# Kernel tuning notes

Hardware: AMD Instinct MI355X
Metric: run time of the kernel (lower is better)

Reference implementation:

```python
import jax, jax.numpy as jnp
import numpy as np

B, C, H, W = 8, 256, 64, 64

def setup_inputs() -> dict:
    key = jax.random.key(0)
    ks = jax.random.split(key, 8)
    s = 0.05  # keep 1x1-conv outputs well-scaled
    return {
        "x": jax.random.normal(ks[0], (B, C, H, W), jnp.float32),
        "Wq": jax.random.normal(ks[1], (C, C), jnp.float32) * s,
        "bq": jax.random.normal(ks[2], (C,), jnp.float32) * s,
        "Wk": jax.random.normal(ks[3], (C, C), jnp.float32) * s,
        "bk": jax.random.normal(ks[4], (C,), jnp.float32) * s,
        "Wv": jax.random.normal(ks[5], (C, C), jnp.float32) * s,
        "bv": jax.random.normal(ks[6], (C,), jnp.float32) * s,
        "gamma": jax.random.normal(ks[7], (1,), jnp.float32),
    }

def reference(x, Wq, bq, Wk, bk, Wv, bv, gamma):
    bs, ch, w, h = x.shape
    n = w * h
    xf = x.reshape(bs, ch, n)                                  # (B, C, N)
    # 1x1 convs == per-position channel matmuls
    q = jnp.einsum('oc,bcn->bon', Wq, xf) + bq[None, :, None]  # (B, C, N)
    k = jnp.einsum('oc,bcn->bon', Wk, xf) + bk[None, :, None]
    v = jnp.einsum('oc,bcn->bon', Wv, xf) + bv[None, :, None]
    # energy[b,i,j] = <q[:,i], k[:,j]>
    energy = jnp.einsum('bci,bcj->bij', q, k)                  # (B, N, N)
    # NOTE: unusual post-softmax scaling by 1/sqrt(N), as in the source
    attn = jax.nn.softmax(energy, axis=-1) / jnp.sqrt(jnp.asarray(n, x.dtype))
    # out[b,c,i] = sum_j v[b,c,j] * attn[b,i,j]
    out = jnp.einsum('bcj,bij->bci', v, attn).reshape(bs, ch, w, h)
    return gamma[0] * out + x
```

## Files before the change

### kernel.cpp

```cpp
#include <hip/hip_runtime.h>

#define B_ 8
#define C_ 256
#define N_ 4096

typedef __attribute__((ext_vector_type(8))) __bf16 bf16x8;
typedef __attribute__((ext_vector_type(4))) float f32x4;

__device__ __forceinline__ unsigned short f2bf(float f) {
  union { float f; unsigned u; } v; v.f = f;
  unsigned r = v.u + 0x7fffu + ((v.u >> 16) & 1u);
  return (unsigned short)(r >> 16);
}

__device__ __forceinline__ uint4 pack8(const float* s) {
  uint4 o;
  o.x = (unsigned)f2bf(s[0]) | ((unsigned)f2bf(s[1]) << 16);
  o.y = (unsigned)f2bf(s[2]) | ((unsigned)f2bf(s[3]) << 16);
  o.z = (unsigned)f2bf(s[4]) | ((unsigned)f2bf(s[5]) << 16);
  o.w = (unsigned)f2bf(s[6]) | ((unsigned)f2bf(s[7]) << 16);
  return o;
}

__device__ __forceinline__ void dma16(const void* g, void* l) {
  __builtin_amdgcn_global_load_lds(
      (const __attribute__((address_space(1))) unsigned int*)(uintptr_t)g,
      (__attribute__((address_space(3))) unsigned int*)(uintptr_t)l, 16, 0, 0);
}

__global__ __launch_bounds__(256) void prep(
    const float* __restrict__ x,
    const float* __restrict__ Wq, const float* __restrict__ Wk,
    const float* __restrict__ Wv,
    unsigned short* __restrict__ xT, unsigned short* __restrict__ Wbf)
{
  __shared__ unsigned int xTl[64][33];
  const int t   = threadIdx.x;
  const int n0  = blockIdx.x * 64;
  const int ct0 = blockIdx.y * 64;
  const int b   = blockIdx.z;

  if (blockIdx.z == 0) {
    const int bid = blockIdx.x + 64 * blockIdx.y;
    if (bid < 96) {
      const int el0 = (bid * 256 + t) * 8;
      const int mat = el0 >> 16;
      const int off = el0 & 65535;
      const float* src = (mat == 0) ? Wq : (mat == 1) ? Wk : Wv;
      float tmp[8];
      float4 f0 = ((const float4*)(src + off))[0];
      float4 f1 = ((const float4*)(src + off))[1];
      tmp[0]=f0.x; tmp[1]=f0.y; tmp[2]=f0.z; tmp[3]=f0.w;
      tmp[4]=f1.x; tmp[5]=f1.y; tmp[6]=f1.z; tmp[7]=f1.w;
      *(uint4*)(Wbf + el0) = pack8(tmp);
    }
  }

  {
    const int cp = t >> 3;
    const int nq = t & 7;
    const float* s0 = x + ((size_t)(b * C_ + ct0 + 2*cp) * N_ + n0 + nq * 8);
    const float* s1 = s0 + N_;
    float4 a0 = ((const float4*)s0)[0], a1 = ((const float4*)s0)[1];
    float4 b0 = ((const float4*)s1)[0], b1 = ((const float4*)s1)[1];
    float lo[8] = {a0.x,a0.y,a0.z,a0.w,a1.x,a1.y,a1.z,a1.w};
    float hi[8] = {b0.x,b0.y,b0.z,b0.w,b1.x,b1.y,b1.z,b1.w};
    #pragma unroll
    for (int k = 0; k < 8; ++k)
      xTl[nq*8 + k][cp] = (unsigned)f2bf(lo[k]) | ((unsigned)f2bf(hi[k]) << 16);
  }
  __syncthreads();

  {
    const int n = t >> 2, cq = t & 3;
    unsigned int vals[8];
    #pragma unroll
    for (int g = 0; g < 8; ++g) vals[g] = xTl[n][cq*8 + g];
    uint4* dst = (uint4*)(xT + ((size_t)(b * N_ + n0 + n)) * C_ + ct0 + cq*16);
    dst[0] = make_uint4(vals[0], vals[1], vals[2], vals[3]);
    dst[1] = make_uint4(vals[4], vals[5], vals[6], vals[7]);
  }
}

__global__ __launch_bounds__(256, 2) void qkv_gemm(
    const unsigned short* __restrict__ xT, const unsigned short* __restrict__ Wbf,
    const float* __restrict__ bq, const float* __restrict__ bk,
    const float* __restrict__ bv,
    unsigned short* __restrict__ qT, unsigned short* __restrict__ kT,
    unsigned short* __restrict__ vW)
{
  __shared__ char smraw[49152];

  const int t    = threadIdx.x;
  const int lane = t & 63;
  const int w    = t >> 6;
  const int m16  = lane & 15;
  const int q    = (lane >> 4) & 3;
  const int nt0  = blockIdx.x * 128;
  const int b    = blockIdx.y;
  const int mat  = blockIdx.z;
  const size_t bN = (size_t)b * N_;

  const unsigned short* Wm = Wbf + mat * 65536;
  const float* bm = (mat == 0) ? bq : (mat == 1) ? bk : bv;
  unsigned short* outp = (mat == 0) ? qT : (mat == 1) ? kT : vW;

  auto stage = [&](int buf, int cs) {
    #pragma unroll
    for (int p = 0; p < 4; ++p) {
      const int row = 64 * w + 16 * p + (lane >> 2);
      const int g   = (lane & 3) ^ (row & 3);
      dma16(Wm + row * 256 + cs * 32 + g * 8,
            smraw + buf * 16384 + (64 * w + 16 * p) * 64);
    }
    #pragma unroll
    for (int p = 0; p < 2; ++p) {
      const int row = 32 * w + 16 * p + (lane >> 2);
      const int g   = (lane & 3) ^ (row & 3);
      dma16(xT + (bN + nt0 + row) * 256 + cs * 32 + g * 8,
            smraw + 32768 + buf * 8192 + (32 * w + 16 * p) * 64);
    }
  };

  stage(0, 0);

  float br[4][4];
  #pragma unroll
  for (int ob = 0; ob < 4; ++ob)
    #pragma unroll
    for (int r = 0; r < 4; ++r) br[ob][r] = bm[64*w + ob*16 + q*4 + r];

  f32x4 acc[4][8] = {};

  for (int cs = 0; cs < 8; ++cs) {
    asm volatile("s_waitcnt vmcnt(0)" ::: "memory");
    __syncthreads();
    if (cs + 1 < 8) stage((cs + 1) & 1, cs + 1);
    const int buf = cs & 1;
    const unsigned short* Wt = (const unsigned short*)(smraw + buf * 16384);
    const unsigned short* Xt = (const unsigned short*)(smraw + 32768 + buf * 8192);

    bf16x8 af[4], bf_[8];
    #pragma unroll
    for (int ob = 0; ob < 4; ++ob) {
      const int o = 64*w + ob*16 + m16;
      af[ob] = *(const bf16x8*)&Wt[o * 32 + ((q ^ (o & 3)) * 8)];
    }
    #pragma unroll
    for (int nb = 0; nb < 8; ++nb) {
      const int n = nb*16 + m16;
      bf_[nb] = *(const bf16x8*)&Xt[n * 32 + ((q ^ (n & 3)) * 8)];
    }
    #pragma unroll
    for (int ob = 0; ob < 4; ++ob)
      #pragma unroll
      for (int nb = 0; nb < 8; ++nb)
        acc[ob][nb] = __builtin_amdgcn_mfma_f32_16x16x32_bf16(af[ob], bf_[nb], acc[ob][nb], 0,0,0);
  }

  float* Dst = (float*)smraw;
  for (int nc = 0; nc < 4; ++nc) {
    __syncthreads();
    #pragma unroll
    for (int ob = 0; ob < 4; ++ob)
      #pragma unroll
      for (int h = 0; h < 2; ++h) {
        const int nb = nc*2 + h;
        #pragma unroll
        for (int r = 0; r < 4; ++r)
          Dst[(64*w + ob*16 + q*4 + r) * 36 + h*16 + m16] = acc[ob][nb][r] + br[ob][r];
      }
    __syncthreads();

    if (mat < 2) {
      const int n_loc = t & 31, oc = t >> 5;
      float vals[32];
      #pragma unroll
      for (int k = 0; k < 32; ++k) vals[k] = Dst[(oc*32 + k) * 36 + n_loc];
      uint4* dst = (uint4*)(outp + (bN + nt0 + nc*32 + n_loc) * C_ + oc*32);
      #pragma unroll
      for (int g = 0; g < 4; ++g) dst[g] = pack8(vals + g*8);
    } else {
      float vals[32], pv[32];
      #pragma unroll
      for (int k = 0; k < 32; ++k) vals[k] = Dst[t * 36 + k];
      #pragma unroll
      for (int p = 0; p < 32; ++p)
        pv[p] = vals[16*((p>>2)&1) + 4*(p>>3) + (p&3)];
      uint4* dst = (uint4*)(outp + ((size_t)(b * C_ + t)) * N_ + nt0 + nc*32);
      #pragma unroll
      for (int g = 0; g < 4; ++g) dst[g] = pack8(pv + g*8);
    }
  }
}

__global__ __launch_bounds__(256, 1) void attn8(
    const unsigned short* __restrict__ qT, const unsigned short* __restrict__ kT,
    const unsigned short* __restrict__ vW, const float* __restrict__ x,
    const float* __restrict__ gamma, float* __restrict__ out)
{
  __shared__ unsigned short Kbuf[2][32 * 256];
  __shared__ unsigned short Vbuf[3][256 * 32];

  const int t    = threadIdx.x;
  const int lane = t & 63;
  const int w    = t >> 6;
  const int b    = blockIdx.x;
  const int i0   = blockIdx.y * 128;
  const int m16  = lane & 15;
  const int q    = (lane >> 4) & 3;
  const int q8   = q * 8;
  const size_t bN = (size_t)b * N_;
  const size_t bC = (size_t)b * C_;

  auto stageK = [&](int buf, int j0) {
    #pragma unroll
    for (int p = 0; p < 4; ++p) {
      const int row = 8*w + 2*p + (lane >> 5);
      const int g   = (lane & 31) ^ (row & 7);
      dma16(kT + (bN + j0 + row) * C_ + g * 8, &Kbuf[buf][(8*w + 2*p) * 256]);
    }
  };
  auto stageV = [&](int buf, int j0) {
    #pragma unroll
    for (int p = 0; p < 4; ++p) {
      const int row = 64*w + 16*p + (lane >> 2);
      const int g   = (lane & 3) ^ ((row >> 1) & 3);
      dma16(vW + (bC + row) * N_ + j0 + g * 8, &Vbuf[buf][(64*w + 16*p) * 32]);
    }
  };

  stageK(0, 0); stageV(0, 0);

  bf16x8 qfA[8], qfB[8];
  {
    const unsigned short* qa = qT + ((bN + i0 + w*32 + m16) * C_ + q8);
    const unsigned short* qb = qa + 16 * C_;
    #pragma unroll
    for (int ks = 0; ks < 8; ++ks) {
      qfA[ks] = *(const bf16x8*)(qa + ks*32);
      qfB[ks] = *(const bf16x8*)(qb + ks*32);
    }
  }

  float lA = 0.0f, lB = 0.0f;
  f32x4 OA[16] = {}, OB[16] = {};
  uint4 pkA, pkB;
  int vb_prev = 0;

  {
    asm volatile("s_waitcnt vmcnt(0)" ::: "memory");
    __syncthreads();
    stageK(1, 32); stageV(1, 32);
    const unsigned short* Kt = Kbuf[0];

    f32x4 sA[2] = {}, sB[2] = {};
    __builtin_amdgcn_s_setprio(1);
    #pragma unroll
    for (int ks = 0; ks < 8; ++ks)
      #pragma unroll
      for (int jb = 0; jb < 2; ++jb) {
        const int j = jb*16 + m16;
        bf16x8 a = *(const bf16x8*)&Kt[j * 256 + (((4*ks + q) ^ (j & 7)) * 8)];
        sA[jb] = __builtin_amdgcn_mfma_f32_16x16x32_bf16(a, qfA[ks], sA[jb], 0,0,0);
        sB[jb] = __builtin_amdgcn_mfma_f32_16x16x32_bf16(a, qfB[ks], sB[jb], 0,0,0);
      }
    __builtin_amdgcn_s_setprio(0);

    float psA[2][4], psB[2][4];
    #pragma unroll
    for (int jb = 0; jb < 2; ++jb)
      #pragma unroll
      for (int r = 0; r < 4; ++r) {
        const float pa = __expf(sA[jb][r] - 64.0f);
        const float pb = __expf(sB[jb][r] - 64.0f);
        psA[jb][r] = pa; lA += pa;
        psB[jb][r] = pb; lB += pb;
      }
    pkA.x = (unsigned)f2bf(psA[0][0]) | ((unsigned)f2bf(psA[0][1]) << 16);
    pkA.y = (unsigned)f2bf(psA[0][2]) | ((unsigned)f2bf(psA[0][3]) << 16);
    pkA.z = (unsigned)f2bf(psA[1][0]) | ((unsigned)f2bf(psA[1][1]) << 16);
    pkA.w = (unsigned)f2bf(psA[1][2]) | ((unsigned)f2bf(psA[1][3]) << 16);
    pkB.x = (unsigned)f2bf(psB[0][0]) | ((unsigned)f2bf(psB[0][1]) << 16);
    pkB.y = (unsigned)f2bf(psB[0][2]) | ((unsigned)f2bf(psB[0][3]) << 16);
    pkB.z = (unsigned)f2bf(psB[1][0]) | ((unsigned)f2bf(psB[1][1]) << 16);
    pkB.w = (unsigned)f2bf(psB[1][2]) | ((unsigned)f2bf(psB[1][3]) << 16);
  }

  for (int jt = 1; jt < 128; ++jt) {
    asm volatile("s_waitcnt vmcnt(0)" ::: "memory");
    __syncthreads();
    const int vb_cur = (vb_prev == 2) ? 0 : vb_prev + 1;
    const int vb_nxt = (vb_cur == 2) ? 0 : vb_cur + 1;
    if (jt + 1 < 128) { stageK((jt + 1) & 1, (jt + 1) * 32); stageV(vb_nxt, (jt + 1) * 32); }

    const unsigned short* Kt = Kbuf[jt & 1];
    const unsigned short* Vp = Vbuf[vb_prev];
    union { uint4 u; bf16x8 v; } pva; pva.u = pkA;
    union { uint4 u; bf16x8 v; } pvb; pvb.u = pkB;

    f32x4 sA[2] = {}, sB[2] = {};
    __builtin_amdgcn_s_setprio(1);
    #pragma unroll
    for (int u = 0; u < 16; ++u) {
      {
        const int ks = u >> 1, jb = u & 1;
        const int j = jb*16 + m16;
        bf16x8 a = *(const bf16x8*)&Kt[j * 256 + (((4*ks + q) ^ (j & 7)) * 8)];
        sA[jb] = __builtin_amdgcn_mfma_f32_16x16x32_bf16(a, qfA[ks], sA[jb], 0,0,0);
        sB[jb] = __builtin_amdgcn_mfma_f32_16x16x32_bf16(a, qfB[ks], sB[jb], 0,0,0);
      }
      {
        const int c = u*16 + m16;
        bf16x8 vf = *(const bf16x8*)&Vp[c * 32 + ((q ^ ((c >> 1) & 3)) * 8)];
        OA[u] = __builtin_amdgcn_mfma_f32_16x16x32_bf16(vf, pva.v, OA[u], 0,0,0);
        OB[u] = __builtin_amdgcn_mfma_f32_16x16x32_bf16(vf, pvb.v, OB[u], 0,0,0);
      }
    }
    __builtin_amdgcn_s_setprio(0);

    float psA[2][4], psB[2][4];
    #pragma unroll
    for (int jb = 0; jb < 2; ++jb)
      #pragma unroll
      for (int r = 0; r < 4; ++r) {
        const float pa = __expf(sA[jb][r] - 64.0f);
        const float pb = __expf(sB[jb][r] - 64.0f);
        psA[jb][r] = pa; lA += pa;
        psB[jb][r] = pb; lB += pb;
      }
    pkA.x = (unsigned)f2bf(psA[0][0]) | ((unsigned)f2bf(psA[0][1]) << 16);
    pkA.y = (unsigned)f2bf(psA[0][2]) | ((unsigned)f2bf(psA[0][3]) << 16);
    pkA.z = (unsigned)f2bf(psA[1][0]) | ((unsigned)f2bf(psA[1][1]) << 16);
    pkA.w = (unsigned)f2bf(psA[1][2]) | ((unsigned)f2bf(psA[1][3]) << 16);
    pkB.x = (unsigned)f2bf(psB[0][0]) | ((unsigned)f2bf(psB[0][1]) << 16);
    pkB.y = (unsigned)f2bf(psB[0][2]) | ((unsigned)f2bf(psB[0][3]) << 16);
    pkB.z = (unsigned)f2bf(psB[1][0]) | ((unsigned)f2bf(psB[1][1]) << 16);
    pkB.w = (unsigned)f2bf(psB[1][2]) | ((unsigned)f2bf(psB[1][3]) << 16);
    vb_prev = vb_cur;
  }

  {
    const unsigned short* Vp = Vbuf[vb_prev];
    union { uint4 u; bf16x8 v; } pva; pva.u = pkA;
    union { uint4 u; bf16x8 v; } pvb; pvb.u = pkB;
    __builtin_amdgcn_s_setprio(1);
    #pragma unroll
    for (int cb = 0; cb < 16; ++cb) {
      const int c = cb*16 + m16;
      bf16x8 vf = *(const bf16x8*)&Vp[c * 32 + ((q ^ ((c >> 1) & 3)) * 8)];
      OA[cb] = __builtin_amdgcn_mfma_f32_16x16x32_bf16(vf, pva.v, OA[cb], 0,0,0);
      OB[cb] = __builtin_amdgcn_mfma_f32_16x16x32_bf16(vf, pvb.v, OB[cb], 0,0,0);
    }
    __builtin_amdgcn_s_setprio(0);
  }

  float lAs = lA;
  lAs += __shfl_xor(lAs, 16);
  lAs += __shfl_xor(lAs, 32);
  float lBs = lB;
  lBs += __shfl_xor(lBs, 16);
  lBs += __shfl_xor(lBs, 32);

  const float gm = gamma[0];
  const float fsA = gm / (lAs * 64.0f);
  const float fsB = gm / (lBs * 64.0f);
  const int icolA = i0 + w*32 + m16;
  const int icolB = icolA + 16;
  #pragma unroll
  for (int cb = 0; cb < 16; ++cb) {
    #pragma unroll
    for (int r = 0; r < 4; ++r) {
      const int c = cb*16 + q*4 + r;
      const size_t idxA = (bC + c) * N_ + icolA;
      out[idxA] = OA[cb][r] * fsA + x[idxA];
      const size_t idxB = idxA + 16;
      out[idxB] = OB[cb][r] * fsB + x[idxB];
    }
  }
}

extern "C" void kernel_launch(void* const* d_in, const int* in_sizes, int n_in,
                              void* d_out, int out_size, void* d_ws, size_t ws_size,
                              hipStream_t stream) {
  const float* x     = (const float*)d_in[0];
  const float* Wq    = (const float*)d_in[1];
  const float* bq    = (const float*)d_in[2];
  const float* Wk    = (const float*)d_in[3];
  const float* bk    = (const float*)d_in[4];
  const float* Wv    = (const float*)d_in[5];
  const float* bv    = (const float*)d_in[6];
  const float* gamma = (const float*)d_in[7];
  float* out = (float*)d_out;

  unsigned short* xT  = (unsigned short*)d_ws;
  unsigned short* Wbf = xT + (size_t)B_ * N_ * C_;
  unsigned short* qT  = Wbf + 3 * 65536;
  unsigned short* kT  = qT + (size_t)B_ * N_ * C_;
  unsigned short* vW  = kT + (size_t)B_ * N_ * C_;

  prep<<<dim3(64, 4, 8), dim3(256), 0, stream>>>(x, Wq, Wk, Wv, xT, Wbf);
  qkv_gemm<<<dim3(32, 8, 3), dim3(256), 0, stream>>>(xT, Wbf, bq, bk, bv, qT, kT, vW);
  attn8<<<dim3(8, 32), dim3(256), 0, stream>>>(qT, kT, vW, x, gamma, out);
}
```

Measured before the change: 331.8 us.

## Split attention key range across two blocks with atomic-flag partial reduction

Splits the key/value loop of each query tile into two halves handled by separate blocks, doubling the grid and allowing two blocks per CU. The first arriving block writes unnormalized partial outputs and row sums to workspace and sets a ready flag; the second spins on it and combines, normalizes and adds the residual. Flags are zeroed in the prep kernel. Also replaces software bf16 rounding with the packed hardware convert instruction. Adds extra global traffic for partials, spin-wait latency, and register pressure from the two-block launch bound.

```diff
diff --git a/kernel.cpp b/kernel.cpp
--- a/kernel.cpp
+++ b/kernel.cpp
@@ -22,6 +22,12 @@
   return o;
 }
 
+__device__ __forceinline__ unsigned cvtpk(float a, float b) {
+  unsigned r;
+  asm("v_cvt_pk_bf16_f32 %0, %1, %2" : "=v"(r) : "v"(a), "v"(b));
+  return r;
+}
+
 __device__ __forceinline__ void dma16(const void* g, void* l) {
   __builtin_amdgcn_global_load_lds(
       (const __attribute__((address_space(1))) unsigned int*)(uintptr_t)g,
@@ -32,7 +38,8 @@
     const float* __restrict__ x,
     const float* __restrict__ Wq, const float* __restrict__ Wk,
     const float* __restrict__ Wv,
-    unsigned short* __restrict__ xT, unsigned short* __restrict__ Wbf)
+    unsigned short* __restrict__ xT, unsigned short* __restrict__ Wbf,
+    unsigned int* __restrict__ flags)
 {
   __shared__ unsigned int xTl[64][33];
   const int t   = threadIdx.x;
@@ -54,6 +61,10 @@
       tmp[4]=f1.x; tmp[5]=f1.y; tmp[6]=f1.z; tmp[7]=f1.w;
       *(uint4*)(Wbf + el0) = pack8(tmp);
     }
+    if (bid == 96) {
+      flags[t] = 0u;
+      flags[256 + t] = 0u;
+    }
   }
 
   {
@@ -194,24 +205,33 @@
   }
 }
 
-__global__ __launch_bounds__(256, 1) void attn8(
+__global__ __launch_bounds__(256, 2) void attn11(
     const unsigned short* __restrict__ qT, const unsigned short* __restrict__ kT,
     const unsigned short* __restrict__ vW, const float* __restrict__ x,
-    const float* __restrict__ gamma, float* __restrict__ out)
+    const float* __restrict__ gamma,
+    float* __restrict__ Opart, float* __restrict__ lpart,
+    unsigned int* __restrict__ arrive, unsigned int* __restrict__ ready,
+    float* __restrict__ out)
 {
   __shared__ unsigned short Kbuf[2][32 * 256];
   __shared__ unsigned short Vbuf[3][256 * 32];
+  __shared__ unsigned int role;
 
   const int t    = threadIdx.x;
   const int lane = t & 63;
   const int w    = t >> 6;
-  const int b    = blockIdx.x;
-  const int i0   = blockIdx.y * 128;
+  const int lin  = blockIdx.x;
+  const int b    = lin & 7;
+  const int itile = (lin >> 3) & 31;
+  const int jh   = lin >> 8;
+  const int i0   = itile * 128;
+  const int jbase = jh * 2048;
   const int m16  = lane & 15;
   const int q    = (lane >> 4) & 3;
   const int q8   = q * 8;
   const size_t bN = (size_t)b * N_;
   const size_t bC = (size_t)b * C_;
+  const int f    = b * 32 + itile;
 
   auto stageK = [&](int buf, int j0) {
     #pragma unroll
@@ -230,7 +250,7 @@
     }
   };
 
-  stageK(0, 0); stageV(0, 0);
+  stageK(0, jbase); stageV(0, jbase);
 
   bf16x8 qfA[8], qfB[8];
   {
@@ -251,7 +271,7 @@
   {
     asm volatile("s_waitcnt vmcnt(0)" ::: "memory");
     __syncthreads();
-    stageK(1, 32); stageV(1, 32);
+    stageK(1, jbase + 32); stageV(1, jbase + 32);
     const unsigned short* Kt = Kbuf[0];
 
     f32x4 sA[2] = {}, sB[2] = {};
@@ -277,22 +297,19 @@
         psA[jb][r] = pa; lA += pa;
         psB[jb][r] = pb; lB += pb;
       }
-    pkA.x = (unsigned)f2bf(psA[0][0]) | ((unsigned)f2bf(psA[0][1]) << 16);
-    pkA.y = (unsigned)f2bf(psA[0][2]) | ((unsigned)f2bf(psA[0][3]) << 16);
-    pkA.z = (unsigned)f2bf(psA[1][0]) | ((unsigned)f2bf(psA[1][1]) << 16);
-    pkA.w = (unsigned)f2bf(psA[1][2]) | ((unsigned)f2bf(psA[1][3]) << 16);
-    pkB.x = (unsigned)f2bf(psB[0][0]) | ((unsigned)f2bf(psB[0][1]) << 16);
-    pkB.y = (unsigned)f2bf(psB[0][2]) | ((unsigned)f2bf(psB[0][3]) << 16);
-    pkB.z = (unsigned)f2bf(psB[1][0]) | ((unsigned)f2bf(psB[1][1]) << 16);
-    pkB.w = (unsigned)f2bf(psB[1][2]) | ((unsigned)f2bf(psB[1][3]) << 16);
-  }
-
-  for (int jt = 1; jt < 128; ++jt) {
+    pkA.x = cvtpk(psA[0][0], psA[0][1]); pkA.y = cvtpk(psA[0][2], psA[0][3]);
+    pkA.z = cvtpk(psA[1][0], psA[1][1]); pkA.w = cvtpk(psA[1][2], psA[1][3]);
+    pkB.x = cvtpk(psB[0][0], psB[0][1]); pkB.y = cvtpk(psB[0][2], psB[0][3]);
+    pkB.z = cvtpk(psB[1][0], psB[1][1]); pkB.w = cvtpk(psB[1][2], psB[1][3]);
+  }
+
+  for (int jt = 1; jt < 64; ++jt) {
     asm volatile("s_waitcnt vmcnt(0)" ::: "memory");
     __syncthreads();
     const int vb_cur = (vb_prev == 2) ? 0 : vb_prev + 1;
     const int vb_nxt = (vb_cur == 2) ? 0 : vb_cur + 1;
-    if (jt + 1 < 128) { stageK((jt + 1) & 1, (jt + 1) * 32); stageV(vb_nxt, (jt + 1) * 32); }
+    if (jt + 1 < 64) { stageK((jt + 1) & 1, jbase + (jt + 1) * 32);
+                       stageV(vb_nxt, jbase + (jt + 1) * 32); }
 
     const unsigned short* Kt = Kbuf[jt & 1];
     const unsigned short* Vp = Vbuf[vb_prev];
@@ -329,14 +346,10 @@
         psA[jb][r] = pa; lA += pa;
         psB[jb][r] = pb; lB += pb;
       }
-    pkA.x = (unsigned)f2bf(psA[0][0]) | ((unsigned)f2bf(psA[0][1]) << 16);
-    pkA.y = (unsigned)f2bf(psA[0][2]) | ((unsigned)f2bf(psA[0][3]) << 16);
-    pkA.z = (unsigned)f2bf(psA[1][0]) | ((unsigned)f2bf(psA[1][1]) << 16);
-    pkA.w = (unsigned)f2bf(psA[1][2]) | ((unsigned)f2bf(psA[1][3]) << 16);
-    pkB.x = (unsigned)f2bf(psB[0][0]) | ((unsigned)f2bf(psB[0][1]) << 16);
-    pkB.y = (unsigned)f2bf(psB[0][2]) | ((unsigned)f2bf(psB[0][3]) << 16);
-    pkB.z = (unsigned)f2bf(psB[1][0]) | ((unsigned)f2bf(psB[1][1]) << 16);
-    pkB.w = (unsigned)f2bf(psB[1][2]) | ((unsigned)f2bf(psB[1][3]) << 16);
+    pkA.x = cvtpk(psA[0][0], psA[0][1]); pkA.y = cvtpk(psA[0][2], psA[0][3]);
+    pkA.z = cvtpk(psA[1][0], psA[1][1]); pkA.w = cvtpk(psA[1][2], psA[1][3]);
+    pkB.x = cvtpk(psB[0][0], psB[0][1]); pkB.y = cvtpk(psB[0][2], psB[0][3]);
+    pkB.z = cvtpk(psB[1][0], psB[1][1]); pkB.w = cvtpk(psB[1][2], psB[1][3]);
     vb_prev = vb_cur;
   }
 
@@ -362,20 +375,49 @@
   lBs += __shfl_xor(lBs, 16);
   lBs += __shfl_xor(lBs, 32);
 
-  const float gm = gamma[0];
-  const float fsA = gm / (lAs * 64.0f);
-  const float fsB = gm / (lBs * 64.0f);
   const int icolA = i0 + w*32 + m16;
-  const int icolB = icolA + 16;
-  #pragma unroll
-  for (int cb = 0; cb < 16; ++cb) {
-    #pragma unroll
-    for (int r = 0; r < 4; ++r) {
-      const int c = cb*16 + q*4 + r;
-      const size_t idxA = (bC + c) * N_ + icolA;
-      out[idxA] = OA[cb][r] * fsA + x[idxA];
-      const size_t idxB = idxA + 16;
-      out[idxB] = OB[cb][r] * fsB + x[idxB];
+
+  __syncthreads();
+  if (t == 0) role = atomicAdd(&arrive[f], 1u);
+  __syncthreads();
+
+  if (role == 0) {
+    if (lane < 16) {
+      lpart[bN + icolA]      = lAs;
+      lpart[bN + icolA + 16] = lBs;
+    }
+    #pragma unroll
+    for (int cb = 0; cb < 16; ++cb) {
+      #pragma unroll
+      for (int r = 0; r < 4; ++r) {
+        const int c = cb*16 + q*4 + r;
+        const size_t idx = (bC + c) * N_ + icolA;
+        Opart[idx]      = OA[cb][r];
+        Opart[idx + 16] = OB[cb][r];
+      }
+    }
+    __syncthreads();
+    if (t == 0)
+      __hip_atomic_store(&ready[f], 1u, __ATOMIC_RELEASE, __HIP_MEMORY_SCOPE_AGENT);
+  } else {
+    while (__hip_atomic_load(&ready[f], __ATOMIC_ACQUIRE,
+                             __HIP_MEMORY_SCOPE_AGENT) == 0u)
+      __builtin_amdgcn_s_sleep(1);
+
+    const float gm  = gamma[0];
+    const float lA2 = lpart[bN + icolA];
+    const float lB2 = lpart[bN + icolA + 16];
+    const float fsA = gm / ((lAs + lA2) * 64.0f);
+    const float fsB = gm / ((lBs + lB2) * 64.0f);
+    #pragma unroll
+    for (int cb = 0; cb < 16; ++cb) {
+      #pragma unroll
+      for (int r = 0; r < 4; ++r) {
+        const int c = cb*16 + q*4 + r;
+        const size_t idx = (bC + c) * N_ + icolA;
+        out[idx]      = (OA[cb][r] + Opart[idx])      * fsA + x[idx];
+        out[idx + 16] = (OB[cb][r] + Opart[idx + 16]) * fsB + x[idx + 16];
+      }
     }
   }
 }
@@ -398,8 +440,13 @@
   unsigned short* qT  = Wbf + 3 * 65536;
   unsigned short* kT  = qT + (size_t)B_ * N_ * C_;
   unsigned short* vW  = kT + (size_t)B_ * N_ * C_;
-
-  prep<<<dim3(64, 4, 8), dim3(256), 0, stream>>>(x, Wq, Wk, Wv, xT, Wbf);
+  float* Opart = (float*)(vW + (size_t)B_ * N_ * C_);
+  float* lpart = Opart + (size_t)B_ * C_ * N_;
+  unsigned int* arrive = (unsigned int*)(lpart + (size_t)B_ * N_);
+  unsigned int* ready  = arrive + 256;
+
+  prep<<<dim3(64, 4, 8), dim3(256), 0, stream>>>(x, Wq, Wk, Wv, xT, Wbf, arrive);
   qkv_gemm<<<dim3(32, 8, 3), dim3(256), 0, stream>>>(xT, Wbf, bq, bk, bv, qT, kT, vW);
-  attn8<<<dim3(8, 32), dim3(256), 0, stream>>>(qT, kT, vW, x, gamma, out);
-}
+  attn11<<<dim3(512), dim3(256), 0, stream>>>(qT, kT, vW, x, gamma,
+                                              Opart, lpart, arrive, ready, out);
+}
```

New measurement: 344.7 us. 3.9% more time.
